# Kernel tuning notes

Hardware: AMD Instinct MI355X
Metric: run time of the kernel (lower is better)

## Reference

```python
import jax, jax.numpy as jnp
import numpy as np
from jax import lax

NMS_THRESH = 0.5
BN_EPS = 1e-5
TO_REMOVE = 1.0  # neural-motifs box convention (+1 in width/height)


def nms_overlaps(boxes):
    # boxes: [N, C, 4] xyxy -> per-class pairwise IoU [N, N, C]
    x1 = jnp.maximum(boxes[:, None, :, 0], boxes[None, :, :, 0])
    y1 = jnp.maximum(boxes[:, None, :, 1], boxes[None, :, :, 1])
    x2 = jnp.minimum(boxes[:, None, :, 2], boxes[None, :, :, 2])
    y2 = jnp.minimum(boxes[:, None, :, 3], boxes[None, :, :, 3])
    inter = jnp.clip(x2 - x1 + TO_REMOVE, 0.0) * jnp.clip(y2 - y1 + TO_REMOVE, 0.0)
    area = (boxes[:, :, 2] - boxes[:, :, 0] + TO_REMOVE) * (boxes[:, :, 3] - boxes[:, :, 1] + TO_REMOVE)  # [N,C]
    union = area[:, None, :] + area[None, :, :] - inter
    return inter / union


def greedy_nms_labels(obj_dists, is_overlap):
    # faithful port of nms_per_cls: iterative argmax + per-class suppression
    N, C = obj_dists.shape
    scores = jax.nn.softmax(obj_dists, axis=-1)
    scores = scores.at[:, 0].set(-1.0)  # kill background column

    def step(carry, _):
        scores, labels = carry
        flat = jnp.argmax(scores)          # row-major, same as np.unravel_index
        box_ind = flat // C
        cls_ind = flat % C
        labels = labels.at[box_ind].set(cls_ind.astype(jnp.int32))
        ov = is_overlap[box_ind, :, cls_ind]  # [N] bool
        col = jnp.where(ov, 0.0, scores[:, cls_ind])
        scores = scores.at[:, cls_ind].set(col)
        scores = scores.at[box_ind, :].set(-1.0)
        return (scores, labels), None

    (_, labels), _ = lax.scan(step, (scores, jnp.zeros(N, jnp.int32)), None, length=N)
    return labels


def setup_inputs() -> dict:
    key = jax.random.key(0)
    ks = jax.random.split(key, 16)
    N, C, D, E, H, P = 400, 151, 4096, 200, 512, 128
    x = jax.random.normal(ks[0], (N, D), jnp.float32)
    predict_logits = jax.random.normal(ks[1], (N, C), jnp.float32) * 2.0
    pos_input = jax.random.uniform(ks[2], (N, 9), jnp.float32)
    xy = jax.random.uniform(ks[3], (N, C, 2), jnp.float32) * 800.0
    wh = jax.random.uniform(ks[4], (N, C, 2), jnp.float32) * 200.0 + 1.0
    boxes_per_cls = jnp.concatenate([xy, xy + wh], axis=-1)
    sc = lambda k, sh: jax.random.normal(k, sh, jnp.float32) * np.float32(1.0 / np.sqrt(sh[0]))
    return {
        'x': x,
        'predict_logits': predict_logits,
        'pos_input': pos_input,
        'boxes_per_cls': boxes_per_cls,
        'obj_embed_w': jax.random.normal(ks[5], (C, E), jnp.float32) * 0.1,
        'obj_embed2_w': jax.random.normal(ks[6], (C, E), jnp.float32) * 0.1,
        'w_pos1': sc(ks[7], (9, 32)), 'b_pos1': jnp.zeros(32, jnp.float32),
        'bn_gamma': jnp.ones(32, jnp.float32), 'bn_beta': jnp.zeros(32, jnp.float32),
        'bn_mean': jnp.zeros(32, jnp.float32), 'bn_var': jnp.ones(32, jnp.float32),
        'w_pos2': sc(ks[8], (32, P)), 'b_pos2': jnp.zeros(P, jnp.float32),
        'w_lin': sc(ks[9], (D + E + P, H)), 'b_lin': jnp.zeros(H, jnp.float32),
        'w_out': sc(ks[10], (H, C)), 'b_out': jnp.zeros(C, jnp.float32),
        'w_fc': sc(ks[11], (D + E + P, H)), 'b_fc': jnp.zeros(H, jnp.float32),
    }


def reference(x, predict_logits, pos_input, boxes_per_cls, obj_embed_w, obj_embed2_w,
              w_pos1, b_pos1, bn_gamma, bn_beta, bn_mean, bn_var, w_pos2, b_pos2,
              w_lin, b_lin, w_out, b_out, w_fc, b_fc):
    # sgdet inference path of VTransEFeaturePE.forward
    obj_embed = jax.nn.softmax(predict_logits, axis=-1) @ obj_embed_w           # [N,E]
    h = pos_input @ w_pos1 + b_pos1                                             # Linear(9,32)
    h = (h - bn_mean) / jnp.sqrt(bn_var + BN_EPS) * bn_gamma + bn_beta          # BN eval
    pos_embed = jax.nn.relu(h @ w_pos2 + b_pos2)                                # [N,128]
    rep = jnp.concatenate([x, obj_embed, pos_embed], axis=-1)                   # [N,4424]
    obj_dists = (rep @ w_lin + b_lin) @ w_out + b_out                           # [N,C]
    is_overlap = nms_overlaps(boxes_per_cls) >= NMS_THRESH                      # [N,N,C]
    obj_preds = greedy_nms_labels(obj_dists, is_overlap)                        # [N] int32
    obj_embed2 = obj_embed2_w[obj_preds]                                        # [N,E]
    obj_rel_rep = jnp.concatenate([x, pos_embed, obj_embed2], axis=-1)
    edge_ctx = jax.nn.relu(obj_rel_rep @ w_fc + b_fc)                           # [N,H]
    return (obj_dists, obj_preds, edge_ctx)
```

## Files before the change

### kernel.cpp

```cpp
#include <hip/hip_runtime.h>
#include <hip/hip_bf16.h>
#include <stdint.h>

#define NB 400
#define NC 151
#define DX 4096
#define DE 200
#define DP 128
#define DH 512
#define KREP 4424
#define TAILW 328
#define MPAD 416
#define SPLITK 8
#define TILES1 139
#define TILES2 132
#define SLOTS 7
#define SKSTRIDE 152

__device__ __forceinline__ uint32_t f2ord(float f) {
  uint32_t u = __float_as_uint(f);
  return (u & 0x80000000u) ? ~u : (u | 0x80000000u);
}

__global__ __launch_bounds__(256) void k_embed(
    const float* __restrict__ logits, const float* __restrict__ obj_embed_w,
    const float* __restrict__ pos_input, const float* __restrict__ w_pos1,
    const float* __restrict__ b_pos1, const float* __restrict__ bn_gamma,
    const float* __restrict__ bn_beta, const float* __restrict__ bn_mean,
    const float* __restrict__ bn_var, const float* __restrict__ w_pos2,
    const float* __restrict__ b_pos2, float* __restrict__ tail1) {
  int r = blockIdx.x, t = threadIdx.x;
  if (r >= NB) {
    if (t < TAILW) tail1[r * TAILW + t] = 0.f;
    return;
  }
  __shared__ float p[NC];
  __shared__ float red[256];
  __shared__ float hb[32];

  float v = (t < NC) ? logits[r * NC + t] : -INFINITY;
  red[t] = v; __syncthreads();
  for (int s = 128; s > 0; s >>= 1) { if (t < s) red[t] = fmaxf(red[t], red[t + s]); __syncthreads(); }
  float m = red[0]; __syncthreads();
  float e = (t < NC) ? expf(v - m) : 0.f;
  red[t] = e; __syncthreads();
  for (int s = 128; s > 0; s >>= 1) { if (t < s) red[t] += red[t + s]; __syncthreads(); }
  float sum = red[0];
  if (t < NC) p[t] = e / sum;

  if (t < 32) {
    float acc = b_pos1[t];
    for (int k = 0; k < 9; k++) acc += pos_input[r * 9 + k] * w_pos1[k * 32 + t];
    acc = (acc - bn_mean[t]) / sqrtf(bn_var[t] + 1e-5f) * bn_gamma[t] + bn_beta[t];
    hb[t] = acc;
  }
  __syncthreads();

  if (t < DE) {
    float acc = 0.f;
    for (int k = 0; k < NC; k++) acc += p[k] * obj_embed_w[k * DE + t];
    tail1[r * TAILW + t] = acc;
  }
  if (t < DP) {
    float acc = b_pos2[t];
    for (int k = 0; k < 32; k++) acc += hb[k] * w_pos2[k * DP + t];
    tail1[r * TAILW + DE + t] = fmaxf(acc, 0.f);
  }
}

__device__ __forceinline__ void gemm_body(
    const float* __restrict__ x, const float* __restrict__ tail,
    const float* __restrict__ w, float* __restrict__ part,
    int bid, int tiles, int toff) {
  __shared__ __align__(16) float As[32][36];
  __shared__ __align__(16) float Bs[32][68];
  int tid = threadIdx.x;
  int n0 = (bid & 7) * 64, m0 = ((bid >> 3) % 13) * 32;
  int z = bid / 104;
  int tbeg = (z * tiles) / SPLITK, tend = ((z + 1) * tiles) / SPLITK;
  int ty = tid >> 4, tx = tid & 15;
  int a_r = tid >> 3, a_c = (tid & 7) << 2;
  int b_r = tid >> 4, b_c = (tid & 15) << 2;
  float4 acc0 = {0, 0, 0, 0}, acc1 = {0, 0, 0, 0};

  auto loadA = [&](int t) -> float4 {
    int k = t * 32 + a_c;
    int row = m0 + a_r;
    float4 v = {0, 0, 0, 0};
    if (k < KREP) {
      if (k < DX) { if (row < NB) v = *(const float4*)&x[(size_t)row * DX + k]; }
      else v = *(const float4*)&tail[row * TAILW + toff + (k - DX)];
    }
    return v;
  };
  auto loadB = [&](int t, int roff) -> float4 {
    int k = t * 32 + b_r + roff;
    float4 v = {0, 0, 0, 0};
    if (k < KREP) v = *(const float4*)&w[(size_t)k * DH + n0 + b_c];
    return v;
  };

  float4 pa = loadA(tbeg), pb0 = loadB(tbeg, 0), pb1 = loadB(tbeg, 16);
  for (int t = tbeg; t < tend; t++) {
    __syncthreads();
    *(float4*)&As[a_r][a_c] = pa;
    *(float4*)&Bs[b_r][b_c] = pb0;
    *(float4*)&Bs[b_r + 16][b_c] = pb1;
    __syncthreads();
    if (t + 1 < tend) { pa = loadA(t + 1); pb0 = loadB(t + 1, 0); pb1 = loadB(t + 1, 16); }
#pragma unroll
    for (int k4 = 0; k4 < 8; k4++) {
      float4 a0 = *(float4*)&As[ty * 2][k4 * 4];
      float4 a1 = *(float4*)&As[ty * 2 + 1][k4 * 4];
#pragma unroll
      for (int j = 0; j < 4; j++) {
        float4 bv = *(float4*)&Bs[k4 * 4 + j][tx * 4];
        float av0 = (&a0.x)[j], av1 = (&a1.x)[j];
        acc0.x += av0 * bv.x; acc0.y += av0 * bv.y; acc0.z += av0 * bv.z; acc0.w += av0 * bv.w;
        acc1.x += av1 * bv.x; acc1.y += av1 * bv.y; acc1.z += av1 * bv.z; acc1.w += av1 * bv.w;
      }
    }
  }
  int row0 = m0 + ty * 2, col = n0 + tx * 4;
  float* base = part + (size_t)z * NB * DH;
  if (row0 < NB)     *(float4*)&base[row0 * DH + col] = acc0;
  if (row0 + 1 < NB) *(float4*)&base[(row0 + 1) * DH + col] = acc1;
}

__global__ __launch_bounds__(256) void k_g1ov(
    const float* __restrict__ x, const float* __restrict__ tail1,
    const float* __restrict__ w_lin, float* __restrict__ part,
    const float* __restrict__ boxes, uint64_t* __restrict__ ov_bits) {
  int bid = blockIdx.x;
  if (bid >= 832) {
    int c = bid - 832;
    int t = threadIdx.x;
    __shared__ float4 bx[NB];
    const float4* bp4 = (const float4*)boxes;
    for (int j = t; j < NB; j += 256) bx[j] = bp4[j * NC + c];
    __syncthreads();
    int wave = t >> 6, lane = t & 63;
    for (int b = wave; b < NB; b += 4) {
      float4 A = bx[b];
      float areaA = (A.z - A.x + 1.f) * (A.w - A.y + 1.f);
      for (int chunk = 0; chunk < 7; chunk++) {
        int j = chunk * 64 + lane;
        bool ov = false;
        if (j < NB) {
          float4 B = bx[j];
          float x1 = fmaxf(A.x, B.x), y1 = fmaxf(A.y, B.y);
          float x2 = fminf(A.z, B.z), y2 = fminf(A.w, B.w);
          float iw = fmaxf(x2 - x1 + 1.f, 0.f), ih = fmaxf(y2 - y1 + 1.f, 0.f);
          float inter = iw * ih;
          float areaB = (B.z - B.x + 1.f) * (B.w - B.y + 1.f);
          ov = (inter / (areaA + areaB - inter)) >= 0.5f;
        }
        uint64_t mask = __ballot(ov);
        if (lane == 0) ov_bits[((size_t)(b * NC + c) << 3) + chunk] = mask;
      }
    }
    return;
  }
  gemm_body(x, tail1, w_lin, part, bid, TILES1, 0);
}

__global__ __launch_bounds__(256) void k_dists(
    const float* __restrict__ part, const float* __restrict__ b_lin,
    const float* __restrict__ w_out, const float* __restrict__ b_out,
    float* __restrict__ out_dists, uint64_t* __restrict__ skeys) {
  int r = blockIdx.x, t = threadIdx.x;
  __shared__ float h[DH];
  __shared__ float red[256];
  __shared__ float sval[NC];
  float s0 = b_lin[t], s1 = b_lin[t + 256];
#pragma unroll
  for (int z = 0; z < SPLITK; z++) {
    const float* pr = part + ((size_t)z * NB + r) * DH;
    s0 += pr[t]; s1 += pr[t + 256];
  }
  h[t] = s0; h[t + 256] = s1;
  __syncthreads();

  float acc = -INFINITY;
  if (t < NC) {
    acc = b_out[t];
    for (int k = 0; k < DH; k++) acc += h[k] * w_out[k * NC + t];
    out_dists[r * NC + t] = acc;
  }
  red[t] = (t < NC) ? acc : -INFINITY; __syncthreads();
  for (int s = 128; s > 0; s >>= 1) { if (t < s) red[t] = fmaxf(red[t], red[t + s]); __syncthreads(); }
  float mx = red[0]; __syncthreads();
  float e = (t < NC) ? expf(acc - mx) : 0.f;
  red[t] = e; __syncthreads();
  for (int s = 128; s > 0; s >>= 1) { if (t < s) red[t] += red[t + s]; __syncthreads(); }
  float sum = red[0];
  if (t < NC) sval[t] = e / sum;
  __syncthreads();

  if (t >= 1 && t < NC) {
    float v = sval[t];
    int rank = 0;
    for (int c2 = 1; c2 < NC; c2++) {
      float v2 = sval[c2];
      rank += (v2 > v) || (v2 == v && c2 < t);
    }
    skeys[(size_t)r * SKSTRIDE + rank] =
        ((uint64_t)f2ord(v) << 17) | ((uint64_t)(511 - r) << 8) | (uint64_t)t;
  }
}

__global__ __launch_bounds__(256) void k_nms_g2a(
    const uint64_t* __restrict__ ov_bits, const uint64_t* __restrict__ skeys,
    int* __restrict__ labels_g, float* __restrict__ out_preds,
    const float* __restrict__ x, const float* __restrict__ tail1,
    const float* __restrict__ w_fc, float* __restrict__ part) {
  if (blockIdx.x > 0) {
    gemm_body(x, tail1, w_fc, part, blockIdx.x - 1, TILES2, DE);
    return;
  }
  if (threadIdx.x >= 64) return;
  int lane = threadIdx.x;
  uint64_t cand[SLOTS];
  uint64_t supp0[SLOTS], supp1[SLOTS], supp2[SLOTS];
  int depth[SLOTS];
  bool removed[SLOTS];
  int reszmin[SLOTS];

#pragma unroll
  for (int s = 0; s < SLOTS; s++) {
    int r = s * 64 + lane;
    supp0[s] = supp1[s] = supp2[s] = 0;
    depth[s] = 0; removed[s] = false; reszmin[s] = 255;
    if (r < NB) {
      cand[s] = skeys[(size_t)r * SKSTRIDE];
      labels_g[r] = 0; out_preds[r] = 0.f;
    } else cand[s] = 0;
  }

  auto apply = [&](int b, int c, const uint64_t* ow) {
#pragma unroll
    for (int s = 0; s < SLOTS; s++) {
      int r = s * 64 + lane;
      if (r == b) {
        removed[s] = true; reszmin[s] = 255;
        cand[s] = ((uint64_t)0x407FFFFFu << 17) | ((uint64_t)(511 - r) << 8);
        labels_g[b] = c; out_preds[b] = (float)c;
      } else if ((ow[s] >> lane) & 1) {
        if (removed[s]) {
          if (c < reszmin[s]) reszmin[s] = c;
          cand[s] = ((uint64_t)0x80000000u << 17) | ((uint64_t)(511 - r) << 8)
                    | (uint64_t)reszmin[s];
        } else {
          uint64_t bit = 1ull << (c & 63);
          if (c < 64) supp0[s] |= bit; else if (c < 128) supp1[s] |= bit; else supp2[s] |= bit;
          if ((int)(cand[s] & 0xFF) == c) {
            int d = depth[s] + 1;
            uint64_t k = 0;
            for (; d < 150; d++) {
              k = skeys[(size_t)r * SKSTRIDE + d];
              int col = (int)(k & 0xFF);
              uint64_t mm = (col < 64) ? supp0[s] : ((col < 128) ? supp1[s] : supp2[s]);
              if (!((mm >> (col & 63)) & 1)) break;
            }
            if (d >= 150)
              k = ((uint64_t)0x80000000u << 17) | ((uint64_t)(511 - r) << 8) | 1ull;
            depth[s] = d; cand[s] = k;
          }
        }
      }
    }
  };

  auto cswap = [](uint64_t& a, uint64_t& b) {
    uint64_t hi = a > b ? a : b, lo = a > b ? b : a; a = hi; b = lo;
  };

  int picked = 0;
  while (picked < NB) {
    uint64_t k0 = 0, k1 = 0, k2 = 0, k3 = 0;
#pragma unroll
    for (int s = 0; s < SLOTS; s++) {
      uint64_t v = cand[s];
      if (v > k0)      { k3 = k2; k2 = k1; k1 = k0; k0 = v; }
      else if (v > k1) { k3 = k2; k2 = k1; k1 = v; }
      else if (v > k2) { k3 = k2; k2 = v; }
      else if (v > k3) { k3 = v; }
    }
#pragma unroll
    for (int off = 1; off < 64; off <<= 1) {
      uint64_t p0 = (uint64_t)__shfl_xor((unsigned long long)k0, off, 64);
      uint64_t p1 = (uint64_t)__shfl_xor((unsigned long long)k1, off, 64);
      uint64_t p2 = (uint64_t)__shfl_xor((unsigned long long)k2, off, 64);
      uint64_t p3 = (uint64_t)__shfl_xor((unsigned long long)k3, off, 64);
      uint64_t t0 = k0 > p3 ? k0 : p3;
      uint64_t t1 = k1 > p2 ? k1 : p2;
      uint64_t t2 = k2 > p1 ? k2 : p1;
      uint64_t t3 = k3 > p0 ? k3 : p0;
      cswap(t0, t2); cswap(t1, t3); cswap(t0, t1); cswap(t2, t3);
      k0 = t0; k1 = t1; k2 = t2; k3 = t3;
    }
    int b0 = 511 - (int)((k0 >> 8) & 0x1FF), c0 = (int)(k0 & 0xFF);
    int b1 = 511 - (int)((k1 >> 8) & 0x1FF), c1 = (int)(k1 & 0xFF);
    int b2 = 511 - (int)((k2 >> 8) & 0x1FF), c2 = (int)(k2 & 0xFF);
    int b3 = 511 - (int)((k3 >> 8) & 0x1FF), c3 = (int)(k3 & 0xFF);
    int npick = NB - picked; if (npick > 4) npick = 4;

    int pi = lane >> 3, pw = lane & 7;
    uint64_t wv = 0;
    if (pi < npick && pw < 7) {
      int bb = (pi == 0) ? b0 : (pi == 1) ? b1 : (pi == 2) ? b2 : b3;
      int cc = (pi == 0) ? c0 : (pi == 1) ? c1 : (pi == 2) ? c2 : c3;
      wv = ov_bits[(((size_t)(bb * NC + cc)) << 3) + pw];
    }
    auto ovb = [&](int ii, int bj) -> bool {
      bool f = ((lane >> 3) == ii) && ((lane & 7) == (bj >> 6)) && ((wv >> (bj & 63)) & 1);
      return __ballot(f) != 0ull;
    };
    uint32_t v1 = (uint32_t)(k1 >> 17), v2 = (uint32_t)(k2 >> 17), v3 = (uint32_t)(k3 >> 17);
    int napply = 1;
    if (npick >= 2 && v1 > 0x80000000u && !(c1 == c0 && ovb(0, b1))) {
      napply = 2;
      if (npick >= 3 && v2 > 0x80000000u &&
          !(c2 == c0 && ovb(0, b2)) && !(c2 == c1 && ovb(1, b2))) {
        napply = 3;
        if (npick >= 4 && v3 > 0x80000000u &&
            !(c3 == c0 && ovb(0, b3)) && !(c3 == c1 && ovb(1, b3)) &&
            !(c3 == c2 && ovb(2, b3)))
          napply = 4;
      }
    }

    uint64_t ow[SLOTS];
#pragma unroll
    for (int s = 0; s < SLOTS; s++) ow[s] = (uint64_t)__shfl((unsigned long long)wv, s, 64);
    apply(b0, c0, ow);
    if (napply >= 2) {
#pragma unroll
      for (int s = 0; s < SLOTS; s++) ow[s] = (uint64_t)__shfl((unsigned long long)wv, 8 + s, 64);
      apply(b1, c1, ow);
    }
    if (napply >= 3) {
#pragma unroll
      for (int s = 0; s < SLOTS; s++) ow[s] = (uint64_t)__shfl((unsigned long long)wv, 16 + s, 64);
      apply(b2, c2, ow);
    }
    if (napply >= 4) {
#pragma unroll
      for (int s = 0; s < SLOTS; s++) ow[s] = (uint64_t)__shfl((unsigned long long)wv, 24 + s, 64);
      apply(b3, c3, ow);
    }
    picked += napply;
  }
}

__global__ __launch_bounds__(256) void k_final(
    const float* __restrict__ emb2, const int* __restrict__ labels,
    const float* __restrict__ w_fc, const float* __restrict__ part,
    const float* __restrict__ b_fc, float* __restrict__ out_edge) {
  __shared__ __align__(16) float As[32][36];
  __shared__ __align__(16) float Bs[32][68];
  int tid = threadIdx.x;
  int n0 = blockIdx.x * 64, m0 = blockIdx.y * 32;
  int ty = tid >> 4, tx = tid & 15;
  int a_r = tid >> 3, a_c = (tid & 7) << 2;
  int b_r = tid >> 4, b_c = (tid & 15) << 2;
  float4 acc0 = {0, 0, 0, 0}, acc1 = {0, 0, 0, 0};
  int row_a = m0 + a_r;
  int lab = (row_a < NB) ? labels[row_a] : 0;

  auto loadA = [&](int t) -> float4 {
    int kk = t * 32 + a_c;
    float4 v = {0, 0, 0, 0};
    if (kk < DE && row_a < NB) v = *(const float4*)&emb2[(size_t)lab * DE + kk];
    return v;
  };
  auto loadB = [&](int t, int roff) -> float4 {
    int kk = t * 32 + b_r + roff;
    float4 v = {0, 0, 0, 0};
    if (kk < DE) v = *(const float4*)&w_fc[(size_t)(DX + DP + kk) * DH + n0 + b_c];
    return v;
  };

  float4 pa = loadA(0), pb0 = loadB(0, 0), pb1 = loadB(0, 16);
  for (int t = 0; t < 7; t++) {
    __syncthreads();
    *(float4*)&As[a_r][a_c] = pa;
    *(float4*)&Bs[b_r][b_c] = pb0;
    *(float4*)&Bs[b_r + 16][b_c] = pb1;
    __syncthreads();
    if (t + 1 < 7) { pa = loadA(t + 1); pb0 = loadB(t + 1, 0); pb1 = loadB(t + 1, 16); }
#pragma unroll
    for (int k4 = 0; k4 < 8; k4++) {
      float4 a0 = *(float4*)&As[ty * 2][k4 * 4];
      float4 a1 = *(float4*)&As[ty * 2 + 1][k4 * 4];
#pragma unroll
      for (int j = 0; j < 4; j++) {
        float4 bv = *(float4*)&Bs[k4 * 4 + j][tx * 4];
        float av0 = (&a0.x)[j], av1 = (&a1.x)[j];
        acc0.x += av0 * bv.x; acc0.y += av0 * bv.y; acc0.z += av0 * bv.z; acc0.w += av0 * bv.w;
        acc1.x += av1 * bv.x; acc1.y += av1 * bv.y; acc1.z += av1 * bv.z; acc1.w += av1 * bv.w;
      }
    }
  }
  int row0 = m0 + ty * 2, col = n0 + tx * 4;
#pragma unroll
  for (int z = 0; z < SPLITK; z++) {
    if (row0 < NB) {
      float4 p = *(const float4*)&part[((size_t)z * NB + row0) * DH + col];
      acc0.x += p.x; acc0.y += p.y; acc0.z += p.z; acc0.w += p.w;
    }
    if (row0 + 1 < NB) {
      float4 p = *(const float4*)&part[((size_t)z * NB + row0 + 1) * DH + col];
      acc1.x += p.x; acc1.y += p.y; acc1.z += p.z; acc1.w += p.w;
    }
  }
  float4 bv = *(const float4*)&b_fc[col];
  if (row0 < NB) {
    float4 r;
    r.x = fmaxf(acc0.x + bv.x, 0.f); r.y = fmaxf(acc0.y + bv.y, 0.f);
    r.z = fmaxf(acc0.z + bv.z, 0.f); r.w = fmaxf(acc0.w + bv.w, 0.f);
    *(float4*)&out_edge[row0 * DH + col] = r;
  }
  if (row0 + 1 < NB) {
    float4 r;
    r.x = fmaxf(acc1.x + bv.x, 0.f); r.y = fmaxf(acc1.y + bv.y, 0.f);
    r.z = fmaxf(acc1.z + bv.z, 0.f); r.w = fmaxf(acc1.w + bv.w, 0.f);
    *(float4*)&out_edge[(row0 + 1) * DH + col] = r;
  }
}

extern "C" void kernel_launch(void* const* d_in, const int* in_sizes, int n_in,
                              void* d_out, int out_size, void* d_ws, size_t ws_size,
                              hipStream_t stream) {
  const float* x            = (const float*)d_in[0];
  const float* logits       = (const float*)d_in[1];
  const float* pos_input    = (const float*)d_in[2];
  const float* boxes        = (const float*)d_in[3];
  const float* obj_embed_w  = (const float*)d_in[4];
  const float* obj_embed2_w = (const float*)d_in[5];
  const float* w_pos1       = (const float*)d_in[6];
  const float* b_pos1       = (const float*)d_in[7];
  const float* bn_gamma     = (const float*)d_in[8];
  const float* bn_beta      = (const float*)d_in[9];
  const float* bn_mean      = (const float*)d_in[10];
  const float* bn_var       = (const float*)d_in[11];
  const float* w_pos2       = (const float*)d_in[12];
  const float* b_pos2       = (const float*)d_in[13];
  const float* w_lin        = (const float*)d_in[14];
  const float* b_lin        = (const float*)d_in[15];
  const float* w_out        = (const float*)d_in[16];
  const float* b_out        = (const float*)d_in[17];
  const float* w_fc         = (const float*)d_in[18];
  const float* b_fc         = (const float*)d_in[19];

  float* ws         = (float*)d_ws;
  float* tail1      = ws;
  int* labels       = (int*)(tail1 + MPAD * TAILW);
  uint64_t* skeys   = (uint64_t*)(labels + MPAD);
  uint64_t* ov_bits = skeys + (size_t)NB * SKSTRIDE;
  float* part       = (float*)(ov_bits + (size_t)NB * NC * 8);

  float* out       = (float*)d_out;
  float* out_dists = out;
  float* out_preds = out + NB * NC;
  float* out_edge  = out + NB * NC + NB;

  k_embed<<<MPAD, 256, 0, stream>>>(logits, obj_embed_w, pos_input, w_pos1, b_pos1,
                                    bn_gamma, bn_beta, bn_mean, bn_var, w_pos2, b_pos2,
                                    tail1);
  k_g1ov<<<983, 256, 0, stream>>>(x, tail1, w_lin, part, boxes, ov_bits);
  k_dists<<<NB, 256, 0, stream>>>(part, b_lin, w_out, b_out, out_dists, skeys);
  k_nms_g2a<<<833, 256, 0, stream>>>(ov_bits, skeys, labels, out_preds,
                                     x, tail1, w_fc, part);
  k_final<<<dim3(8, 13), 256, 0, stream>>>(obj_embed2_w, labels, w_fc, part,
                                           b_fc, out_edge);
}
```

Measured before the change: 628.1 us.

## Widen greedy NMS batch to eight picks per round and cache sorted keys in LDS

```diff
diff --git a/kernel.cpp b/kernel.cpp
--- a/kernel.cpp
+++ b/kernel.cpp
@@ -16,6 +16,7 @@
 #define TILES2 132
 #define SLOTS 7
 #define SKSTRIDE 152
+#define SKPRE 12
 
 __device__ __forceinline__ uint32_t f2ord(float f) {
   uint32_t u = __float_as_uint(f);
@@ -218,6 +219,15 @@
     gemm_body(x, tail1, w_fc, part, blockIdx.x - 1, TILES2, DE);
     return;
   }
+  __shared__ uint64_t skc[NB][SKPRE];
+  {
+    int t = threadIdx.x;
+    for (int i = t; i < NB * SKPRE; i += 256) {
+      int r = i / SKPRE, d = i - r * SKPRE;
+      skc[r][d] = skeys[(size_t)r * SKSTRIDE + d];
+    }
+  }
+  __syncthreads();
   if (threadIdx.x >= 64) return;
   int lane = threadIdx.x;
   uint64_t cand[SLOTS];
@@ -232,122 +242,135 @@
     supp0[s] = supp1[s] = supp2[s] = 0;
     depth[s] = 0; removed[s] = false; reszmin[s] = 255;
     if (r < NB) {
-      cand[s] = skeys[(size_t)r * SKSTRIDE];
+      cand[s] = skc[r][0];
       labels_g[r] = 0; out_preds[r] = 0.f;
     } else cand[s] = 0;
   }
 
-  auto apply = [&](int b, int c, const uint64_t* ow) {
+  auto CE = [](uint64_t& a, uint64_t& b) {
+    uint64_t hi = a > b ? a : b, lo = a > b ? b : a; a = hi; b = lo;
+  };
+
+  int picked = 0;
+  while (picked < NB) {
+    uint64_t tk[8];
+#pragma unroll
+    for (int i = 0; i < SLOTS; i++) tk[i] = cand[i];
+    tk[7] = 0;
+    CE(tk[0],tk[1]); CE(tk[2],tk[3]); CE(tk[4],tk[5]); CE(tk[6],tk[7]);
+    CE(tk[0],tk[2]); CE(tk[1],tk[3]); CE(tk[4],tk[6]); CE(tk[5],tk[7]);
+    CE(tk[1],tk[2]); CE(tk[5],tk[6]); CE(tk[0],tk[4]); CE(tk[3],tk[7]);
+    CE(tk[1],tk[5]); CE(tk[2],tk[6]);
+    CE(tk[1],tk[4]); CE(tk[3],tk[6]);
+    CE(tk[2],tk[4]); CE(tk[3],tk[5]);
+    CE(tk[3],tk[4]);
+
+#pragma unroll
+    for (int off = 1; off < 64; off <<= 1) {
+      uint64_t p[8];
+#pragma unroll
+      for (int i = 0; i < 8; i++)
+        p[i] = (uint64_t)__shfl_xor((unsigned long long)tk[i], off, 64);
+      uint64_t m[8];
+#pragma unroll
+      for (int i = 0; i < 8; i++) m[i] = tk[i] > p[7 - i] ? tk[i] : p[7 - i];
+      CE(m[0],m[4]); CE(m[1],m[5]); CE(m[2],m[6]); CE(m[3],m[7]);
+      CE(m[0],m[2]); CE(m[1],m[3]); CE(m[4],m[6]); CE(m[5],m[7]);
+      CE(m[0],m[1]); CE(m[2],m[3]); CE(m[4],m[5]); CE(m[6],m[7]);
+#pragma unroll
+      for (int i = 0; i < 8; i++) tk[i] = m[i];
+    }
+
+    int npick = NB - picked; if (npick > 8) npick = 8;
+
+    int pi = lane >> 3, pw = lane & 7;
+    int bsel = 0, csel = 0;
+#pragma unroll
+    for (int i = 0; i < 8; i++)
+      if (pi == i) {
+        bsel = 511 - (int)((tk[i] >> 8) & 0x1FF);
+        csel = (int)(tk[i] & 0xFF);
+      }
+    uint64_t wv = 0;
+    if (pi < npick && pw < 7)
+      wv = ov_bits[(((size_t)(bsel * NC + csel)) << 3) + pw];
+
+    uint64_t balnz_raw = __ballot(wv != 0ull);
+
+    uint64_t ovall = 0;
+#pragma unroll
+    for (int j = 0; j < 8; j++) {
+      int bj = 511 - (int)((tk[j] >> 8) & 0x1FF);
+      bool hit = (pw == (bj >> 6)) && ((wv >> (bj & 63)) & 1);
+      uint64_t bal = __ballot(hit);
+      bal |= bal >> 4; bal |= bal >> 2; bal |= bal >> 1;
+      uint32_t m8 = (uint32_t)(((bal & 0x0101010101010101ULL) * 0x0102040810204080ULL) >> 56);
+      ovall |= (uint64_t)m8 << (8 * j);
+    }
+
+    int napply = 1; bool stop = false;
+#pragma unroll
+    for (int j = 1; j < 8; j++) {
+      bool bad = (j >= npick) || ((uint32_t)(tk[j] >> 17) <= 0x80000000u);
+      int cj = (int)(tk[j] & 0xFF);
+#pragma unroll
+      for (int i = 0; i < j; i++)
+        bad = bad || (((int)(tk[i] & 0xFF) == cj) && ((ovall >> (8 * j + i)) & 1));
+      stop = stop || bad;
+      if (!stop) napply = j + 1;
+    }
+
+    uint64_t am = (napply >= 8) ? ~0ull : ((1ull << (8 * napply)) - 1);
+    uint64_t balnz = balnz_raw & am;
+    uint32_t bslots = 0;
+#pragma unroll
+    for (int i = 0; i < 8; i++)
+      if (i < napply) bslots |= 1u << ((511 - (int)((tk[i] >> 8) & 0x1FF)) >> 6);
+
 #pragma unroll
     for (int s = 0; s < SLOTS; s++) {
+      bool touched = (((balnz >> s) & 0x0101010101010101ULL) != 0) || ((bslots >> s) & 1);
+      if (!touched) continue;
+      uint64_t ow[8];
+#pragma unroll
+      for (int i = 0; i < 8; i++)
+        ow[i] = (i < napply) ? (uint64_t)__shfl((unsigned long long)wv, i * 8 + s, 64) : 0;
       int r = s * 64 + lane;
-      if (r == b) {
-        removed[s] = true; reszmin[s] = 255;
-        cand[s] = ((uint64_t)0x407FFFFFu << 17) | ((uint64_t)(511 - r) << 8);
-        labels_g[b] = c; out_preds[b] = (float)c;
-      } else if ((ow[s] >> lane) & 1) {
-        if (removed[s]) {
-          if (c < reszmin[s]) reszmin[s] = c;
-          cand[s] = ((uint64_t)0x80000000u << 17) | ((uint64_t)(511 - r) << 8)
-                    | (uint64_t)reszmin[s];
-        } else {
-          uint64_t bit = 1ull << (c & 63);
-          if (c < 64) supp0[s] |= bit; else if (c < 128) supp1[s] |= bit; else supp2[s] |= bit;
-          if ((int)(cand[s] & 0xFF) == c) {
-            int d = depth[s] + 1;
-            uint64_t k = 0;
-            for (; d < 150; d++) {
-              k = skeys[(size_t)r * SKSTRIDE + d];
-              int col = (int)(k & 0xFF);
-              uint64_t mm = (col < 64) ? supp0[s] : ((col < 128) ? supp1[s] : supp2[s]);
-              if (!((mm >> (col & 63)) & 1)) break;
+#pragma unroll
+      for (int i = 0; i < 8; i++) {
+        if (i < napply) {
+          int b = 511 - (int)((tk[i] >> 8) & 0x1FF);
+          int c = (int)(tk[i] & 0xFF);
+          uint64_t owv = ow[i];
+          if (r == b) {
+            removed[s] = true; reszmin[s] = 255;
+            cand[s] = ((uint64_t)0x407FFFFFu << 17) | ((uint64_t)(511 - r) << 8);
+            labels_g[b] = c; out_preds[b] = (float)c;
+          } else if ((owv >> lane) & 1) {
+            if (removed[s]) {
+              if (c < reszmin[s]) reszmin[s] = c;
+              cand[s] = ((uint64_t)0x80000000u << 17) | ((uint64_t)(511 - r) << 8)
+                        | (uint64_t)reszmin[s];
+            } else {
+              uint64_t bit = 1ull << (c & 63);
+              if (c < 64) supp0[s] |= bit; else if (c < 128) supp1[s] |= bit; else supp2[s] |= bit;
+              if ((int)(cand[s] & 0xFF) == c) {
+                int d = depth[s] + 1;
+                uint64_t k = 0;
+                for (; d < 150; d++) {
+                  k = (d < SKPRE) ? skc[r][d] : skeys[(size_t)r * SKSTRIDE + d];
+                  int col = (int)(k & 0xFF);
+                  uint64_t mm = (col < 64) ? supp0[s] : ((col < 128) ? supp1[s] : supp2[s]);
+                  if (!((mm >> (col & 63)) & 1)) break;
+                }
+                if (d >= 150)
+                  k = ((uint64_t)0x80000000u << 17) | ((uint64_t)(511 - r) << 8) | 1ull;
+                depth[s] = d; cand[s] = k;
+              }
             }
-            if (d >= 150)
-              k = ((uint64_t)0x80000000u << 17) | ((uint64_t)(511 - r) << 8) | 1ull;
-            depth[s] = d; cand[s] = k;
           }
         }
       }
-    }
-  };
-
-  auto cswap = [](uint64_t& a, uint64_t& b) {
-    uint64_t hi = a > b ? a : b, lo = a > b ? b : a; a = hi; b = lo;
-  };
-
-  int picked = 0;
-  while (picked < NB) {
-    uint64_t k0 = 0, k1 = 0, k2 = 0, k3 = 0;
-#pragma unroll
-    for (int s = 0; s < SLOTS; s++) {
-      uint64_t v = cand[s];
-      if (v > k0)      { k3 = k2; k2 = k1; k1 = k0; k0 = v; }
-      else if (v > k1) { k3 = k2; k2 = k1; k1 = v; }
-      else if (v > k2) { k3 = k2; k2 = v; }
-      else if (v > k3) { k3 = v; }
-    }
-#pragma unroll
-    for (int off = 1; off < 64; off <<= 1) {
-      uint64_t p0 = (uint64_t)__shfl_xor((unsigned long long)k0, off, 64);
-      uint64_t p1 = (uint64_t)__shfl_xor((unsigned long long)k1, off, 64);
-      uint64_t p2 = (uint64_t)__shfl_xor((unsigned long long)k2, off, 64);
-      uint64_t p3 = (uint64_t)__shfl_xor((unsigned long long)k3, off, 64);
-      uint64_t t0 = k0 > p3 ? k0 : p3;
-      uint64_t t1 = k1 > p2 ? k1 : p2;
-      uint64_t t2 = k2 > p1 ? k2 : p1;
-      uint64_t t3 = k3 > p0 ? k3 : p0;
-      cswap(t0, t2); cswap(t1, t3); cswap(t0, t1); cswap(t2, t3);
-      k0 = t0; k1 = t1; k2 = t2; k3 = t3;
-    }
-    int b0 = 511 - (int)((k0 >> 8) & 0x1FF), c0 = (int)(k0 & 0xFF);
-    int b1 = 511 - (int)((k1 >> 8) & 0x1FF), c1 = (int)(k1 & 0xFF);
-    int b2 = 511 - (int)((k2 >> 8) & 0x1FF), c2 = (int)(k2 & 0xFF);
-    int b3 = 511 - (int)((k3 >> 8) & 0x1FF), c3 = (int)(k3 & 0xFF);
-    int npick = NB - picked; if (npick > 4) npick = 4;
-
-    int pi = lane >> 3, pw = lane & 7;
-    uint64_t wv = 0;
-    if (pi < npick && pw < 7) {
-      int bb = (pi == 0) ? b0 : (pi == 1) ? b1 : (pi == 2) ? b2 : b3;
-      int cc = (pi == 0) ? c0 : (pi == 1) ? c1 : (pi == 2) ? c2 : c3;
-      wv = ov_bits[(((size_t)(bb * NC + cc)) << 3) + pw];
-    }
-    auto ovb = [&](int ii, int bj) -> bool {
-      bool f = ((lane >> 3) == ii) && ((lane & 7) == (bj >> 6)) && ((wv >> (bj & 63)) & 1);
-      return __ballot(f) != 0ull;
-    };
-    uint32_t v1 = (uint32_t)(k1 >> 17), v2 = (uint32_t)(k2 >> 17), v3 = (uint32_t)(k3 >> 17);
-    int napply = 1;
-    if (npick >= 2 && v1 > 0x80000000u && !(c1 == c0 && ovb(0, b1))) {
-      napply = 2;
-      if (npick >= 3 && v2 > 0x80000000u &&
-          !(c2 == c0 && ovb(0, b2)) && !(c2 == c1 && ovb(1, b2))) {
-        napply = 3;
-        if (npick >= 4 && v3 > 0x80000000u &&
-            !(c3 == c0 && ovb(0, b3)) && !(c3 == c1 && ovb(1, b3)) &&
-            !(c3 == c2 && ovb(2, b3)))
-          napply = 4;
-      }
-    }
-
-    uint64_t ow[SLOTS];
-#pragma unroll
-    for (int s = 0; s < SLOTS; s++) ow[s] = (uint64_t)__shfl((unsigned long long)wv, s, 64);
-    apply(b0, c0, ow);
-    if (napply >= 2) {
-#pragma unroll
-      for (int s = 0; s < SLOTS; s++) ow[s] = (uint64_t)__shfl((unsigned long long)wv, 8 + s, 64);
-      apply(b1, c1, ow);
-    }
-    if (napply >= 3) {
-#pragma unroll
-      for (int s = 0; s < SLOTS; s++) ow[s] = (uint64_t)__shfl((unsigned long long)wv, 16 + s, 64);
-      apply(b2, c2, ow);
-    }
-    if (napply >= 4) {
-#pragma unroll
-      for (int s = 0; s < SLOTS; s++) ow[s] = (uint64_t)__shfl((unsigned long long)wv, 24 + s, 64);
-      apply(b3, c3, ow);
     }
     picked += napply;
   }
```

New measurement: 994.3 us. 58.3% more time.

## Spread greedy NMS across four waves with shared-memory top-4 merge

Applied to the files above, without the earlier changes.

```diff
diff --git a/kernel.cpp b/kernel.cpp
--- a/kernel.cpp
+++ b/kernel.cpp
@@ -14,7 +14,6 @@
 #define SPLITK 8
 #define TILES1 139
 #define TILES2 132
-#define SLOTS 7
 #define SKSTRIDE 152
 
 __device__ __forceinline__ uint32_t f2ord(float f) {
@@ -69,11 +68,10 @@
 }
 
 __device__ __forceinline__ void gemm_body(
+    float (*As)[36], float (*Bs)[68],
     const float* __restrict__ x, const float* __restrict__ tail,
     const float* __restrict__ w, float* __restrict__ part,
     int bid, int tiles, int toff) {
-  __shared__ __align__(16) float As[32][36];
-  __shared__ __align__(16) float Bs[32][68];
   int tid = threadIdx.x;
   int n0 = (bid & 7) * 64, m0 = ((bid >> 3) % 13) * 32;
   int z = bid / 104;
@@ -131,6 +129,8 @@
     const float* __restrict__ x, const float* __restrict__ tail1,
     const float* __restrict__ w_lin, float* __restrict__ part,
     const float* __restrict__ boxes, uint64_t* __restrict__ ov_bits) {
+  __shared__ __align__(16) float As[32][36];
+  __shared__ __align__(16) float Bs[32][68];
   int bid = blockIdx.x;
   if (bid >= 832) {
     int c = bid - 832;
@@ -161,7 +161,7 @@
     }
     return;
   }
-  gemm_body(x, tail1, w_lin, part, bid, TILES1, 0);
+  gemm_body(As, Bs, x, tail1, w_lin, part, bid, TILES1, 0);
 }
 
 __global__ __launch_bounds__(256) void k_dists(
@@ -209,83 +209,57 @@
   }
 }
 
+struct GemmSm { float As[32][36]; float Bs[32][68]; };
+struct NmsSm  { uint64_t top4[4][4]; uint64_t ovw[4][8]; int nap; };
+
 __global__ __launch_bounds__(256) void k_nms_g2a(
     const uint64_t* __restrict__ ov_bits, const uint64_t* __restrict__ skeys,
     int* __restrict__ labels_g, float* __restrict__ out_preds,
     const float* __restrict__ x, const float* __restrict__ tail1,
     const float* __restrict__ w_fc, float* __restrict__ part) {
+  __shared__ __align__(16) union { GemmSm g; NmsSm n; } sm;
   if (blockIdx.x > 0) {
-    gemm_body(x, tail1, w_fc, part, blockIdx.x - 1, TILES2, DE);
+    gemm_body(sm.g.As, sm.g.Bs, x, tail1, w_fc, part, blockIdx.x - 1, TILES2, DE);
     return;
   }
-  if (threadIdx.x >= 64) return;
-  int lane = threadIdx.x;
-  uint64_t cand[SLOTS];
-  uint64_t supp0[SLOTS], supp1[SLOTS], supp2[SLOTS];
-  int depth[SLOTS];
-  bool removed[SLOTS];
-  int reszmin[SLOTS];
-
-#pragma unroll
-  for (int s = 0; s < SLOTS; s++) {
-    int r = s * 64 + lane;
-    supp0[s] = supp1[s] = supp2[s] = 0;
-    depth[s] = 0; removed[s] = false; reszmin[s] = 255;
+  int tid = threadIdx.x, wave = tid >> 6, lane = tid & 63;
+  int S0w = wave * 2;
+  uint64_t cand[2];
+  uint64_t supp0[2], supp1[2], supp2[2];
+  int depth[2];
+  bool removed[2];
+  int reszmin[2];
+
+#pragma unroll
+  for (int u = 0; u < 2; u++) {
+    int r = (S0w + u) * 64 + lane;
+    supp0[u] = supp1[u] = supp2[u] = 0;
+    depth[u] = 0; removed[u] = false; reszmin[u] = 255;
     if (r < NB) {
-      cand[s] = skeys[(size_t)r * SKSTRIDE];
+      cand[u] = skeys[(size_t)r * SKSTRIDE];
       labels_g[r] = 0; out_preds[r] = 0.f;
-    } else cand[s] = 0;
-  }
-
-  auto apply = [&](int b, int c, const uint64_t* ow) {
-#pragma unroll
-    for (int s = 0; s < SLOTS; s++) {
-      int r = s * 64 + lane;
-      if (r == b) {
-        removed[s] = true; reszmin[s] = 255;
-        cand[s] = ((uint64_t)0x407FFFFFu << 17) | ((uint64_t)(511 - r) << 8);
-        labels_g[b] = c; out_preds[b] = (float)c;
-      } else if ((ow[s] >> lane) & 1) {
-        if (removed[s]) {
-          if (c < reszmin[s]) reszmin[s] = c;
-          cand[s] = ((uint64_t)0x80000000u << 17) | ((uint64_t)(511 - r) << 8)
-                    | (uint64_t)reszmin[s];
-        } else {
-          uint64_t bit = 1ull << (c & 63);
-          if (c < 64) supp0[s] |= bit; else if (c < 128) supp1[s] |= bit; else supp2[s] |= bit;
-          if ((int)(cand[s] & 0xFF) == c) {
-            int d = depth[s] + 1;
-            uint64_t k = 0;
-            for (; d < 150; d++) {
-              k = skeys[(size_t)r * SKSTRIDE + d];
-              int col = (int)(k & 0xFF);
-              uint64_t mm = (col < 64) ? supp0[s] : ((col < 128) ? supp1[s] : supp2[s]);
-              if (!((mm >> (col & 63)) & 1)) break;
-            }
-            if (d >= 150)
-              k = ((uint64_t)0x80000000u << 17) | ((uint64_t)(511 - r) << 8) | 1ull;
-            depth[s] = d; cand[s] = k;
-          }
-        }
-      }
-    }
-  };
+    } else cand[u] = 0;
+  }
 
   auto cswap = [](uint64_t& a, uint64_t& b) {
     uint64_t hi = a > b ? a : b, lo = a > b ? b : a; a = hi; b = lo;
   };
+  auto merge4 = [&](uint64_t a0, uint64_t a1, uint64_t a2, uint64_t a3,
+                    uint64_t e0, uint64_t e1, uint64_t e2, uint64_t e3,
+                    uint64_t& o0, uint64_t& o1, uint64_t& o2, uint64_t& o3) {
+    uint64_t m0 = a0 > e3 ? a0 : e3;
+    uint64_t m1 = a1 > e2 ? a1 : e2;
+    uint64_t m2 = a2 > e1 ? a2 : e1;
+    uint64_t m3 = a3 > e0 ? a3 : e0;
+    cswap(m0, m2); cswap(m1, m3); cswap(m0, m1); cswap(m2, m3);
+    o0 = m0; o1 = m1; o2 = m2; o3 = m3;
+  };
 
   int picked = 0;
   while (picked < NB) {
-    uint64_t k0 = 0, k1 = 0, k2 = 0, k3 = 0;
-#pragma unroll
-    for (int s = 0; s < SLOTS; s++) {
-      uint64_t v = cand[s];
-      if (v > k0)      { k3 = k2; k2 = k1; k1 = k0; k0 = v; }
-      else if (v > k1) { k3 = k2; k2 = k1; k1 = v; }
-      else if (v > k2) { k3 = k2; k2 = v; }
-      else if (v > k3) { k3 = v; }
-    }
+    uint64_t k0 = cand[0] > cand[1] ? cand[0] : cand[1];
+    uint64_t k1 = cand[0] > cand[1] ? cand[1] : cand[0];
+    uint64_t k2 = 0, k3 = 0;
 #pragma unroll
     for (int off = 1; off < 64; off <<= 1) {
       uint64_t p0 = (uint64_t)__shfl_xor((unsigned long long)k0, off, 64);
@@ -299,55 +273,97 @@
       cswap(t0, t2); cswap(t1, t3); cswap(t0, t1); cswap(t2, t3);
       k0 = t0; k1 = t1; k2 = t2; k3 = t3;
     }
-    int b0 = 511 - (int)((k0 >> 8) & 0x1FF), c0 = (int)(k0 & 0xFF);
-    int b1 = 511 - (int)((k1 >> 8) & 0x1FF), c1 = (int)(k1 & 0xFF);
-    int b2 = 511 - (int)((k2 >> 8) & 0x1FF), c2 = (int)(k2 & 0xFF);
-    int b3 = 511 - (int)((k3 >> 8) & 0x1FF), c3 = (int)(k3 & 0xFF);
+    if (lane < 4) {
+      uint64_t kv = (lane == 0) ? k0 : (lane == 1) ? k1 : (lane == 2) ? k2 : k3;
+      sm.n.top4[wave][lane] = kv;
+    }
+    __syncthreads();
+
+    uint64_t A0 = sm.n.top4[0][0], A1 = sm.n.top4[0][1], A2 = sm.n.top4[0][2], A3 = sm.n.top4[0][3];
+    uint64_t B0 = sm.n.top4[1][0], B1 = sm.n.top4[1][1], B2 = sm.n.top4[1][2], B3 = sm.n.top4[1][3];
+    uint64_t C0 = sm.n.top4[2][0], C1 = sm.n.top4[2][1], C2 = sm.n.top4[2][2], C3 = sm.n.top4[2][3];
+    uint64_t D0 = sm.n.top4[3][0], D1 = sm.n.top4[3][1], D2 = sm.n.top4[3][2], D3 = sm.n.top4[3][3];
+    uint64_t P0, P1, P2, P3, Q0, Q1, Q2, Q3, g0, g1, g2, g3;
+    merge4(A0, A1, A2, A3, B0, B1, B2, B3, P0, P1, P2, P3);
+    merge4(C0, C1, C2, C3, D0, D1, D2, D3, Q0, Q1, Q2, Q3);
+    merge4(P0, P1, P2, P3, Q0, Q1, Q2, Q3, g0, g1, g2, g3);
+
+    int b0 = 511 - (int)((g0 >> 8) & 0x1FF), c0 = (int)(g0 & 0xFF);
+    int b1 = 511 - (int)((g1 >> 8) & 0x1FF), c1 = (int)(g1 & 0xFF);
+    int b2 = 511 - (int)((g2 >> 8) & 0x1FF), c2 = (int)(g2 & 0xFF);
+    int b3 = 511 - (int)((g3 >> 8) & 0x1FF), c3 = (int)(g3 & 0xFF);
     int npick = NB - picked; if (npick > 4) npick = 4;
 
-    int pi = lane >> 3, pw = lane & 7;
-    uint64_t wv = 0;
-    if (pi < npick && pw < 7) {
-      int bb = (pi == 0) ? b0 : (pi == 1) ? b1 : (pi == 2) ? b2 : b3;
-      int cc = (pi == 0) ? c0 : (pi == 1) ? c1 : (pi == 2) ? c2 : c3;
-      wv = ov_bits[(((size_t)(bb * NC + cc)) << 3) + pw];
-    }
-    auto ovb = [&](int ii, int bj) -> bool {
-      bool f = ((lane >> 3) == ii) && ((lane & 7) == (bj >> 6)) && ((wv >> (bj & 63)) & 1);
-      return __ballot(f) != 0ull;
-    };
-    uint32_t v1 = (uint32_t)(k1 >> 17), v2 = (uint32_t)(k2 >> 17), v3 = (uint32_t)(k3 >> 17);
-    int napply = 1;
-    if (npick >= 2 && v1 > 0x80000000u && !(c1 == c0 && ovb(0, b1))) {
-      napply = 2;
-      if (npick >= 3 && v2 > 0x80000000u &&
-          !(c2 == c0 && ovb(0, b2)) && !(c2 == c1 && ovb(1, b2))) {
-        napply = 3;
-        if (npick >= 4 && v3 > 0x80000000u &&
-            !(c3 == c0 && ovb(0, b3)) && !(c3 == c1 && ovb(1, b3)) &&
-            !(c3 == c2 && ovb(2, b3)))
-          napply = 4;
-      }
-    }
-
-    uint64_t ow[SLOTS];
-#pragma unroll
-    for (int s = 0; s < SLOTS; s++) ow[s] = (uint64_t)__shfl((unsigned long long)wv, s, 64);
-    apply(b0, c0, ow);
-    if (napply >= 2) {
-#pragma unroll
-      for (int s = 0; s < SLOTS; s++) ow[s] = (uint64_t)__shfl((unsigned long long)wv, 8 + s, 64);
-      apply(b1, c1, ow);
-    }
-    if (napply >= 3) {
-#pragma unroll
-      for (int s = 0; s < SLOTS; s++) ow[s] = (uint64_t)__shfl((unsigned long long)wv, 16 + s, 64);
-      apply(b2, c2, ow);
-    }
-    if (napply >= 4) {
-#pragma unroll
-      for (int s = 0; s < SLOTS; s++) ow[s] = (uint64_t)__shfl((unsigned long long)wv, 24 + s, 64);
-      apply(b3, c3, ow);
+    if (wave == 0) {
+      int pi = lane >> 3, pw = lane & 7;
+      uint64_t wv = 0;
+      if (pi < npick && pw < 7) {
+        int bb = (pi == 0) ? b0 : (pi == 1) ? b1 : (pi == 2) ? b2 : b3;
+        int cc = (pi == 0) ? c0 : (pi == 1) ? c1 : (pi == 2) ? c2 : c3;
+        wv = ov_bits[(((size_t)(bb * NC + cc)) << 3) + pw];
+      }
+      auto ovb = [&](int ii, int bj) -> bool {
+        bool f = ((lane >> 3) == ii) && ((lane & 7) == (bj >> 6)) && ((wv >> (bj & 63)) & 1);
+        return __ballot(f) != 0ull;
+      };
+      uint32_t v1 = (uint32_t)(g1 >> 17), v2 = (uint32_t)(g2 >> 17), v3 = (uint32_t)(g3 >> 17);
+      int napl = 1;
+      if (npick >= 2 && v1 > 0x80000000u && !(c1 == c0 && ovb(0, b1))) {
+        napl = 2;
+        if (npick >= 3 && v2 > 0x80000000u &&
+            !(c2 == c0 && ovb(0, b2)) && !(c2 == c1 && ovb(1, b2))) {
+          napl = 3;
+          if (npick >= 4 && v3 > 0x80000000u &&
+              !(c3 == c0 && ovb(0, b3)) && !(c3 == c1 && ovb(1, b3)) &&
+              !(c3 == c2 && ovb(2, b3)))
+            napl = 4;
+        }
+      }
+      if (lane < 32) sm.n.ovw[pi][pw] = wv;
+      if (lane == 0) sm.n.nap = napl;
+    }
+    __syncthreads();
+    int napply = sm.n.nap;
+
+#pragma unroll
+    for (int u = 0; u < 2; u++) {
+      int S = S0w + u;
+      int r = S * 64 + lane;
+#pragma unroll
+      for (int i = 0; i < 4; i++) {
+        if (i < napply) {
+          int b = (i == 0) ? b0 : (i == 1) ? b1 : (i == 2) ? b2 : b3;
+          int c = (i == 0) ? c0 : (i == 1) ? c1 : (i == 2) ? c2 : c3;
+          uint64_t owv = sm.n.ovw[i][S];
+          if (r == b) {
+            removed[u] = true; reszmin[u] = 255;
+            cand[u] = ((uint64_t)0x407FFFFFu << 17) | ((uint64_t)(511 - r) << 8);
+            labels_g[b] = c; out_preds[b] = (float)c;
+          } else if ((owv >> lane) & 1) {
+            if (removed[u]) {
+              if (c < reszmin[u]) reszmin[u] = c;
+              cand[u] = ((uint64_t)0x80000000u << 17) | ((uint64_t)(511 - r) << 8)
+                        | (uint64_t)reszmin[u];
+            } else {
+              uint64_t bit = 1ull << (c & 63);
+              if (c < 64) supp0[u] |= bit; else if (c < 128) supp1[u] |= bit; else supp2[u] |= bit;
+              if ((int)(cand[u] & 0xFF) == c) {
+                int d = depth[u] + 1;
+                uint64_t k = 0;
+                for (; d < 150; d++) {
+                  k = skeys[(size_t)r * SKSTRIDE + d];
+                  int col = (int)(k & 0xFF);
+                  uint64_t mm = (col < 64) ? supp0[u] : ((col < 128) ? supp1[u] : supp2[u]);
+                  if (!((mm >> (col & 63)) & 1)) break;
+                }
+                if (d >= 150)
+                  k = ((uint64_t)0x80000000u << 17) | ((uint64_t)(511 - r) << 8) | 1ull;
+                depth[u] = d; cand[u] = k;
+              }
+            }
+          }
+        }
+      }
     }
     picked += napply;
   }
```

New measurement: 595.8 us. -5.1%, faster.
